# Kernel optimization log

Measured on AMD Instinct MI355X. Metric: run time of the kernel, lower is better.

## Reference

```python
import jax, jax.numpy as jnp
import numpy as np

N, M, E, DIM = 100000, 2000, 400000, 128
GIN = 2 * DIM + 3  # gate MLP input width


def _mlp2(x, W1, b1, W2, b2):
    # Linear -> ReLU -> Linear
    return jnp.maximum(x @ W1 + b1, 0.0) @ W2 + b2


def setup_inputs() -> dict:
    key = jax.random.key(0)
    ks = jax.random.split(key, 20)
    s = lambda fan_in: 1.0 / np.sqrt(fan_in)
    inp = {
        "res_feat": jax.random.normal(ks[0], (N, DIM), jnp.float32),
        "meta_feat": jax.random.normal(ks[1], (M, DIM), jnp.float32),
        "sec_ids": jax.random.randint(ks[2], (N,), 0, M),
        "batch_pe_vector": jax.random.normal(ks[3], (N, 3), jnp.float32),
        "batch_meta_2_node_edge": jax.random.randint(ks[4], (2, E), 0, M),
        "batch_meta_2_node_vector": jax.random.normal(ks[5], (E, 3), jnp.float32),
        # gate1 params
        "g1_W1": jax.random.uniform(ks[6], (GIN, DIM), jnp.float32, -s(GIN), s(GIN)),
        "g1_b1": jnp.zeros((DIM,), jnp.float32),
        "g1_W2": jax.random.uniform(ks[7], (DIM, DIM), jnp.float32, -s(DIM), s(DIM)),
        "g1_b2": jnp.zeros((DIM,), jnp.float32),
        # gate2 params
        "g2_W1": jax.random.uniform(ks[8], (GIN, DIM), jnp.float32, -s(GIN), s(GIN)),
        "g2_b1": jnp.zeros((DIM,), jnp.float32),
        "g2_W2": jax.random.uniform(ks[9], (DIM, DIM), jnp.float32, -s(DIM), s(DIM)),
        "g2_b2": jnp.zeros((DIM,), jnp.float32),
        # fuse params
        "f_W1": jax.random.uniform(ks[10], (DIM, DIM), jnp.float32, -s(DIM), s(DIM)),
        "f_b1": jnp.zeros((DIM,), jnp.float32),
        "f_W2": jax.random.uniform(ks[11], (DIM, DIM), jnp.float32, -s(DIM), s(DIM)),
        "f_b2": jnp.zeros((DIM,), jnp.float32),
    }
    return inp


def reference(res_feat, meta_feat, sec_ids, batch_pe_vector,
              batch_meta_2_node_edge, batch_meta_2_node_vector,
              g1_W1, g1_b1, g1_W2, g1_b2,
              g2_W1, g2_b1, g2_W2, g2_b2,
              f_W1, f_b1, f_W2, f_b2):
    n = res_feat.shape[0]
    # gate1: per-node gather of meta features
    meta_broadcast = meta_feat[sec_ids]                       # [N, dim]
    gate1_in = jnp.concatenate([res_feat, meta_broadcast, -batch_pe_vector], axis=-1)
    gate1_w = _mlp2(gate1_in, g1_W1, g1_b1, g1_W2, g1_b2)     # [N, dim]
    # gate2: per-edge gathers
    src, dst = batch_meta_2_node_edge[0], batch_meta_2_node_edge[1]
    meta_add = meta_feat[src]                                 # [E, dim]
    res_b = res_feat[dst]                                     # [E, dim]
    gate2_in = jnp.concatenate([res_b, meta_add, batch_meta_2_node_vector], axis=-1)
    gate2_w = _mlp2(gate2_in, g2_W1, g2_b1, g2_W2, g2_b2)     # [E, dim]
    # scatter_mean over destination nodes
    vals = gate2_w * meta_add
    sums = jax.ops.segment_sum(vals, dst, num_segments=n)
    cnts = jax.ops.segment_sum(jnp.ones((vals.shape[0],), vals.dtype), dst, num_segments=n)
    meta_add_fea = sums / jnp.maximum(cnts, 1.0)[:, None]
    fused = res_feat + gate1_w * meta_broadcast + meta_add_fea
    return _mlp2(fused, f_W1, f_b1, f_W2, f_b2)
```

## Files before the change

kernel.cpp:

```cpp
#include <hip/hip_runtime.h>


typedef short bf16x8 __attribute__((ext_vector_type(8)));
typedef float f32x4  __attribute__((ext_vector_type(4)));

#define XS_PAD 136

__device__ __forceinline__ unsigned short f2bf(float f){
  union { float f; unsigned u; } v; v.f = f;
  return (unsigned short)((v.u + 0x7FFFu + ((v.u >> 16) & 1u)) >> 16);
}
__device__ __forceinline__ unsigned pack2(float a, float b){
  return (unsigned)f2bf(a) | ((unsigned)f2bf(b) << 16);
}

__device__ __forceinline__ void mfma_layer(const unsigned short* Xs,
                                           const bf16x8 (&B)[2][4],
                                           int lane, f32x4 (&acc)[4][2]) {
  const int lcol = lane & 15, quad = lane >> 4;
  #pragma unroll
  for (int rg = 0; rg < 4; ++rg) {
    bf16x8 A[4];
    const unsigned short* ab = Xs + (rg*16 + lcol)*XS_PAD + quad*8;
    #pragma unroll
    for (int kk = 0; kk < 4; ++kk) A[kk] = *(const bf16x8*)(ab + kk*32);
    #pragma unroll
    for (int ctl = 0; ctl < 2; ++ctl)
      #pragma unroll
      for (int kk = 0; kk < 4; ++kk)
        acc[rg][ctl] = __builtin_amdgcn_mfma_f32_16x16x32_bf16(
            A[kk], B[ctl][kk], acc[rg][ctl], 0, 0, 0);
  }
}

__device__ __forceinline__ void load_bfrags(const unsigned short* __restrict__ Wt,
                                            int wave, int lane, bf16x8 (&B)[2][4]) {
  const int lcol = lane & 15, quad = lane >> 4;
  #pragma unroll
  for (int ctl = 0; ctl < 2; ++ctl) {
    int col = (wave*2 + ctl)*16 + lcol;
    #pragma unroll
    for (int kk = 0; kk < 4; ++kk)
      B[ctl][kk] = *(const bf16x8*)(Wt + (size_t)col*128 + kk*32 + quad*8);
  }
}

__device__ __forceinline__ void zero_acc(f32x4 (&acc)[4][2]) {
  #pragma unroll
  for (int rg = 0; rg < 4; ++rg)
    #pragma unroll
    for (int ctl = 0; ctl < 2; ++ctl) {
      acc[rg][ctl][0]=0.f; acc[rg][ctl][1]=0.f;
      acc[rg][ctl][2]=0.f; acc[rg][ctl][3]=0.f;
    }
}

struct WPtrs { const float* s[8]; };
__global__ __launch_bounds__(256) void transpose_w8(WPtrs p,
                                                    unsigned short* __restrict__ dstbase,
                                                    int* __restrict__ counts, int M) {
  int slab = blockIdx.x >> 4, blk = blockIdx.x & 15;
  const float* W = p.s[slab];
  unsigned short* Wt = dstbase + (size_t)slab*16384;
  int c  = blk*8 + (threadIdx.x >> 5);
  int k0 = (threadIdx.x & 31) * 4;
  unsigned short o[4];
  #pragma unroll
  for (int j = 0; j < 4; ++j) o[j] = f2bf(W[(size_t)(k0 + j)*128 + c]);
  *(uint2*)(Wt + (size_t)c*128 + k0) =
      make_uint2((unsigned)o[0] | ((unsigned)o[1] << 16),
                 (unsigned)o[2] | ((unsigned)o[3] << 16));
  int tid = blockIdx.x*256 + threadIdx.x;
  int tot = gridDim.x*256;
  for (int i = tid; i < M; i += tot) counts[i] = 0;
}

__global__ __launch_bounds__(256) void prep_and_hist(
    const float* __restrict__ res, const float* __restrict__ meta,
    const unsigned short* __restrict__ WAt, const unsigned short* __restrict__ WBt,
    const float* __restrict__ b1,
    float* __restrict__ A2, float* __restrict__ M2, int mrows, int nbPrep,
    const int* __restrict__ dst, int* __restrict__ counts, int E) {
  if ((int)blockIdx.x >= nbPrep) {
    int e = ((int)blockIdx.x - nbPrep)*256 + threadIdx.x;
    if (e < E) atomicAdd(&counts[dst[e]], 1);
    return;
  }
  __shared__ __align__(16) unsigned short Xs[64*XS_PAD];
  const int t = threadIdx.x, lane = t & 63, wave = t >> 6;
  const int quad = lane >> 4, lcol = lane & 15;
  const int half = nbPrep >> 1;
  const int yy = ((int)blockIdx.x >= half) ? 1 : 0;
  const int bx = (int)blockIdx.x - yy*half;
  const int tile0 = bx * 64;
  const float* X = yy ? meta : res;
  const unsigned short* Wt = yy ? WBt : WAt;
  float* Y = yy ? M2 : A2;
  bf16x8 B[2][4];
  load_bfrags(Wt, wave, lane, B);
  #pragma unroll
  for (int i = 0; i < 8; ++i) {
    int f = t + i*256, row = f >> 5, c4 = f & 31;
    int gr = tile0 + row;
    float4 v = make_float4(0.f,0.f,0.f,0.f);
    if (gr < mrows) v = *(const float4*)(X + (size_t)gr*128 + c4*4);
    *(uint2*)(Xs + row*XS_PAD + c4*4) = make_uint2(pack2(v.x,v.y), pack2(v.z,v.w));
  }
  __syncthreads();
  f32x4 acc[4][2]; zero_acc(acc);
  mfma_layer(Xs, B, lane, acc);
  #pragma unroll
  for (int rg = 0; rg < 4; ++rg)
    #pragma unroll
    for (int ctl = 0; ctl < 2; ++ctl) {
      int col = (wave*2 + ctl)*16 + lcol;
      float badd = 0.f;
      if (!yy) badd = b1[col];
      #pragma unroll
      for (int reg = 0; reg < 4; ++reg) {
        int gr = tile0 + rg*16 + quad*4 + reg;
        if (gr < mrows) Y[(size_t)gr*128 + col] = acc[rg][ctl][reg] + badd;
      }
    }
}

__global__ __launch_bounds__(1024) void scan_all(const int* __restrict__ counts,
                                                 int* __restrict__ row_start,
                                                 int* __restrict__ cursor, int M) {
  __shared__ int s[1024];
  __shared__ int carry_s;
  const int t = threadIdx.x;
  if (t == 0) carry_s = 0;
  __syncthreads();
  for (int base = 0; base < M; base += 2048) {
    int i0 = base + 2*t, i1 = i0 + 1;
    int c0 = (i0 < M) ? counts[i0] : 0;
    int c1 = (i1 < M) ? counts[i1] : 0;
    int pair = c0 + c1;
    s[t] = pair; __syncthreads();
    for (int off = 1; off < 1024; off <<= 1) {
      int x = (t >= off) ? s[t-off] : 0; __syncthreads();
      s[t] += x; __syncthreads();
    }
    int carry = carry_s;
    int excl = carry + s[t] - pair;
    if (i0 < M) { row_start[i0] = excl;       cursor[i0] = excl; }
    if (i1 < M) { row_start[i1] = excl + c0;  cursor[i1] = excl + c0; }
    __syncthreads();
    if (t == 1023) carry_s = carry + s[1023];
    __syncthreads();
  }
}

__global__ void fill_kernel(const int* __restrict__ dst, const int* __restrict__ src,
                            const float* __restrict__ evec, int* __restrict__ cursor,
                            float4* __restrict__ edata, int E) {
  int e = blockIdx.x*256 + threadIdx.x;
  if (e < E) {
    int p = atomicAdd(&cursor[dst[e]], 1);
    edata[p] = make_float4(__int_as_float(src[e]),
                           evec[(size_t)e*3], evec[(size_t)e*3+1], evec[(size_t)e*3+2]);
  }
}

__global__ __launch_bounds__(256) void edge_mfma(
    const float* __restrict__ A2, const float* __restrict__ M2,
    const float* __restrict__ meta, const float4* __restrict__ edata,
    const int* __restrict__ row_start, const int* __restrict__ counts,
    const float* __restrict__ g2W1full,
    const unsigned short* __restrict__ W2t, const float* __restrict__ b2,
    float* __restrict__ SUM) {
  const int n = blockIdx.x;
  const int cnt = counts[n];
  if (cnt <= 0) return;
  const int rs = row_start[n];

  __shared__ __align__(16) unsigned short Xh[64*XS_PAD];
  __shared__ int srcl[64];
  __shared__ float evl[192];
  const int t = threadIdx.x, lane = t & 63, wave = t >> 6;
  const int quad = lane >> 4, lcol = lane & 15;
  const int c0 = (t & 31) * 4, rbase = t >> 5;

  float4 ed = make_float4(0.f,0.f,0.f,0.f);
  if (t < 64 && t < cnt) ed = edata[rs + t];

  bf16x8 BW2[2][4];
  load_bfrags(W2t, wave, lane, BW2);
  float4 base = *(const float4*)(A2 + (size_t)n*128 + c0);
  float4 w0 = *(const float4*)(g2W1full + 256*128 + c0);
  float4 w1 = *(const float4*)(g2W1full + 257*128 + c0);
  float4 w2 = *(const float4*)(g2W1full + 258*128 + c0);
  const int colA = wave*32 + lcol, colB = colA + 16;
  const float b2A = b2[colA], b2B = b2[colB];
  float psA = 0.f, psB = 0.f;

  for (int t0 = 0; t0 < cnt; t0 += 64) {
    if (t0) __syncthreads();
    if (t < 64) {
      srcl[t] = __float_as_int(ed.x);
      evl[3*t] = ed.y; evl[3*t+1] = ed.z; evl[3*t+2] = ed.w;
      int idx = t0 + 64 + t;
      ed = make_float4(0.f,0.f,0.f,0.f);
      if (idx < cnt) ed = edata[rs + idx];
    }
    __syncthreads();
    #pragma unroll
    for (int i = 0; i < 8; ++i) {
      int row = rbase + 8*i;
      float4 h = make_float4(0.f,0.f,0.f,0.f);
      if (t0 + row < cnt) {
        int s = srcl[row];
        float4 m = *(const float4*)(M2 + (size_t)s*128 + c0);
        float e0 = evl[3*row], e1 = evl[3*row+1], e2 = evl[3*row+2];
        h.x = fmaxf(base.x + m.x + e0*w0.x + e1*w1.x + e2*w2.x, 0.f);
        h.y = fmaxf(base.y + m.y + e0*w0.y + e1*w1.y + e2*w2.y, 0.f);
        h.z = fmaxf(base.z + m.z + e0*w0.z + e1*w1.z + e2*w2.z, 0.f);
        h.w = fmaxf(base.w + m.w + e0*w0.w + e1*w1.w + e2*w2.w, 0.f);
      }
      *(uint2*)(Xh + row*XS_PAD + c0) = make_uint2(pack2(h.x,h.y), pack2(h.z,h.w));
    }
    __syncthreads();
    f32x4 acc[4][2]; zero_acc(acc);
    mfma_layer(Xh, BW2, lane, acc);
    #pragma unroll
    for (int rg = 0; rg < 4; ++rg)
      #pragma unroll
      for (int reg = 0; reg < 4; ++reg) {
        int rl = rg*16 + quad*4 + reg;
        if (t0 + rl < cnt) {
          int s = srcl[rl];
          psA += (acc[rg][0][reg] + b2A) * meta[(size_t)s*128 + colA];
          psB += (acc[rg][1][reg] + b2B) * meta[(size_t)s*128 + colB];
        }
      }
  }
  psA += __shfl_xor(psA, 16, 64); psA += __shfl_xor(psA, 32, 64);
  psB += __shfl_xor(psB, 16, 64); psB += __shfl_xor(psB, 32, 64);
  if (quad == 0) {
    SUM[(size_t)n*128 + colA] = psA;
    SUM[(size_t)n*128 + colB] = psB;
  }
}

__global__ __launch_bounds__(256) void fused_node(
    const float* __restrict__ res, const float* __restrict__ meta,
    const int* __restrict__ sec_ids, const float* __restrict__ pe,
    const float* __restrict__ g1W1full,
    const unsigned short* __restrict__ g1At, const unsigned short* __restrict__ g1Bt,
    const unsigned short* __restrict__ g1W2t, const float* __restrict__ g1b1,
    const float* __restrict__ g1b2,
    const unsigned short* __restrict__ fW1t, const float* __restrict__ fb1v,
    const unsigned short* __restrict__ fW2t, const float* __restrict__ fb2v,
    const float* __restrict__ SUM, const int* __restrict__ counts, int msize,
    float* __restrict__ out, int rows) {
  __shared__ __align__(16) unsigned short Xs[64*XS_PAD];
  __shared__ int   sids[64];
  __shared__ float pel[192];
  __shared__ float inv[64];
  const int t = threadIdx.x, lane = t & 63, wave = t >> 6;
  const int quad = lane >> 4, lcol = lane & 15;
  const int tile0 = blockIdx.x * 64;
  const int c0 = (t & 31) * 4, rbase = t >> 5;
  const int colA = wave*32 + lcol, colB = colA + 16;

  if (t < 64) {
    int gr = tile0 + t;
    sids[t] = (gr < rows) ? sec_ids[gr] : 0;
    float p0=0.f,p1=0.f,p2=0.f;
    if (gr < rows){ p0=pe[(size_t)gr*3]; p1=pe[(size_t)gr*3+1]; p2=pe[(size_t)gr*3+2]; }
    pel[3*t]=p0; pel[3*t+1]=p1; pel[3*t+2]=p2;
    int c = (gr < rows && gr < msize) ? counts[gr] : 0;
    inv[t] = (c > 0) ? 1.f/(float)c : 0.f;
  }
  bf16x8 BF[2][4];
  load_bfrags(g1At, wave, lane, BF);
  #pragma unroll
  for (int i = 0; i < 8; ++i) {
    int row = rbase + 8*i, gr = tile0 + row;
    float4 v = make_float4(0.f,0.f,0.f,0.f);
    if (gr < rows) v = *(const float4*)(res + (size_t)gr*128 + c0);
    *(uint2*)(Xs + row*XS_PAD + c0) = make_uint2(pack2(v.x,v.y), pack2(v.z,v.w));
  }
  __syncthreads();
  f32x4 acc[4][2]; zero_acc(acc);
  mfma_layer(Xs, BF, lane, acc);
  load_bfrags(g1Bt, wave, lane, BF);
  __syncthreads();
  #pragma unroll
  for (int i = 0; i < 8; ++i) {
    int row = rbase + 8*i, gr = tile0 + row;
    float4 v = make_float4(0.f,0.f,0.f,0.f);
    if (gr < rows) v = *(const float4*)(meta + (size_t)sids[row]*128 + c0);
    *(uint2*)(Xs + row*XS_PAD + c0) = make_uint2(pack2(v.x,v.y), pack2(v.z,v.w));
  }
  __syncthreads();
  mfma_layer(Xs, BF, lane, acc);
  load_bfrags(g1W2t, wave, lane, BF);
  __syncthreads();
  {
    const float b1A = g1b1[colA], b1B = g1b1[colB];
    const float wA0 = g1W1full[256*128+colA], wA1 = g1W1full[257*128+colA],
                wA2 = g1W1full[258*128+colA];
    const float wB0 = g1W1full[256*128+colB], wB1 = g1W1full[257*128+colB],
                wB2 = g1W1full[258*128+colB];
    #pragma unroll
    for (int rg = 0; rg < 4; ++rg)
      #pragma unroll
      for (int reg = 0; reg < 4; ++reg) {
        int row = rg*16 + quad*4 + reg;
        float p0 = pel[3*row], p1 = pel[3*row+1], p2 = pel[3*row+2];
        float vA = acc[rg][0][reg] + b1A - p0*wA0 - p1*wA1 - p2*wA2;
        float vB = acc[rg][1][reg] + b1B - p0*wB0 - p1*wB1 - p2*wB2;
        Xs[row*XS_PAD + colA] = f2bf(fmaxf(vA, 0.f));
        Xs[row*XS_PAD + colB] = f2bf(fmaxf(vB, 0.f));
      }
  }
  __syncthreads();
  zero_acc(acc);
  mfma_layer(Xs, BF, lane, acc);
  load_bfrags(fW1t, wave, lane, BF);
  __syncthreads();
  {
    const float b2A = g1b2[colA], b2B = g1b2[colB];
    #pragma unroll
    for (int rg = 0; rg < 4; ++rg)
      #pragma unroll
      for (int reg = 0; reg < 4; ++reg) {
        int row = rg*16 + quad*4 + reg, gr = tile0 + row;
        unsigned short oA = 0, oB = 0;
        if (gr < rows) {
          int sid = sids[row];
          float gA = acc[rg][0][reg] + b2A, gB = acc[rg][1][reg] + b2B;
          float mA = meta[(size_t)sid*128 + colA], mB = meta[(size_t)sid*128 + colB];
          float rA = res[(size_t)gr*128 + colA],  rB = res[(size_t)gr*128 + colB];
          float iv = inv[row];
          float sA = 0.f, sB = 0.f;
          if (iv > 0.f) {
            sA = SUM[(size_t)gr*128 + colA] * iv;
            sB = SUM[(size_t)gr*128 + colB] * iv;
          }
          oA = f2bf(rA + gA*mA + sA);
          oB = f2bf(rB + gB*mB + sB);
        }
        Xs[row*XS_PAD + colA] = oA;
        Xs[row*XS_PAD + colB] = oB;
      }
  }
  __syncthreads();
  zero_acc(acc);
  mfma_layer(Xs, BF, lane, acc);
  load_bfrags(fW2t, wave, lane, BF);
  __syncthreads();
  {
    const float fb1A = fb1v[colA], fb1B = fb1v[colB];
    #pragma unroll
    for (int rg = 0; rg < 4; ++rg)
      #pragma unroll
      for (int reg = 0; reg < 4; ++reg) {
        int row = rg*16 + quad*4 + reg;
        Xs[row*XS_PAD + colA] = f2bf(fmaxf(acc[rg][0][reg] + fb1A, 0.f));
        Xs[row*XS_PAD + colB] = f2bf(fmaxf(acc[rg][1][reg] + fb1B, 0.f));
      }
  }
  __syncthreads();
  zero_acc(acc);
  mfma_layer(Xs, BF, lane, acc);
  {
    const float fb2A = fb2v[colA], fb2B = fb2v[colB];
    #pragma unroll
    for (int rg = 0; rg < 4; ++rg)
      #pragma unroll
      for (int reg = 0; reg < 4; ++reg) {
        int gr = tile0 + rg*16 + quad*4 + reg;
        if (gr < rows) {
          out[(size_t)gr*128 + colA] = acc[rg][0][reg] + fb2A;
          out[(size_t)gr*128 + colB] = acc[rg][1][reg] + fb2B;
        }
      }
  }
}

extern "C" void kernel_launch(void* const* d_in, const int* in_sizes, int n_in,
                              void* d_out, int out_size, void* d_ws, size_t ws_size,
                              hipStream_t stream) {
  const float* res     = (const float*)d_in[0];
  const float* meta    = (const float*)d_in[1];
  const int*   sec_ids = (const int*)  d_in[2];
  const float* pe      = (const float*)d_in[3];
  const int*   edge    = (const int*)  d_in[4];
  const float* evec    = (const float*)d_in[5];
  const float* g1W1 = (const float*)d_in[6];
  const float* g1b1 = (const float*)d_in[7];
  const float* g1W2 = (const float*)d_in[8];
  const float* g1b2 = (const float*)d_in[9];
  const float* g2W1 = (const float*)d_in[10];
  const float* g2b1 = (const float*)d_in[11];
  const float* g2W2 = (const float*)d_in[12];
  const float* g2b2 = (const float*)d_in[13];
  const float* fW1  = (const float*)d_in[14];
  const float* fb1  = (const float*)d_in[15];
  const float* fW2  = (const float*)d_in[16];
  const float* fb2  = (const float*)d_in[17];

  const int N = in_sizes[0] / 128;
  const int M = in_sizes[1] / 128;
  const int E = in_sizes[4] / 2;
  const int* src = edge;
  const int* dst = edge + E;

  float* ws = (float*)d_ws;
  float* A2   = ws;
  float* M2   = A2 + (size_t)M*128;
  float* SUMb = M2 + (size_t)M*128;
  int* counts     = (int*)(SUMb + (size_t)M*128);
  int* row_startp = counts + M;
  int* cursor     = row_startp + M;
  uintptr_t ap = (uintptr_t)(cursor + M);
  ap = (ap + 15) & ~(uintptr_t)15;
  float4* edata = (float4*)ap;
  uintptr_t wp = (uintptr_t)(edata + E);
  wp = (wp + 15) & ~(uintptr_t)15;
  unsigned short* Wt = (unsigned short*)wp;
  unsigned short* W_g1A  = Wt + 0*16384;
  unsigned short* W_g1B  = Wt + 1*16384;
  unsigned short* W_g1W2 = Wt + 2*16384;
  unsigned short* W_g2A  = Wt + 3*16384;
  unsigned short* W_g2B  = Wt + 4*16384;
  unsigned short* W_g2W2 = Wt + 5*16384;
  unsigned short* W_fW1  = Wt + 6*16384;
  unsigned short* W_fW2  = Wt + 7*16384;
  float* out = (float*)d_out;

  WPtrs p;
  p.s[0] = g1W1;            p.s[1] = g1W1 + 128*128;  p.s[2] = g1W2;
  p.s[3] = g2W1;            p.s[4] = g2W1 + 128*128;  p.s[5] = g2W2;
  p.s[6] = fW1;             p.s[7] = fW2;

  const int nbMt = (M + 63) / 64;
  const int nbN  = (N + 63) / 64;
  const int nbE  = (E + 255) / 256;
  const int nbPrep = 2*nbMt;

  transpose_w8<<<128, 256, 0, stream>>>(p, Wt, counts, M);
  prep_and_hist<<<nbPrep + nbE, 256, 0, stream>>>(res, meta, W_g2A, W_g2B, g2b1,
                                                  A2, M2, M, nbPrep, dst, counts, E);
  scan_all<<<1, 1024, 0, stream>>>(counts, row_startp, cursor, M);
  fill_kernel<<<nbE, 256, 0, stream>>>(dst, src, evec, cursor, edata, E);
  edge_mfma<<<M, 256, 0, stream>>>(A2, M2, meta, edata, row_startp, counts,
                                   g2W1, W_g2W2, g2b2, SUMb);
  fused_node<<<nbN, 256, 0, stream>>>(res, meta, sec_ids, pe, g1W1,
                                      W_g1A, W_g1B, W_g1W2, g1b1, g1b2,
                                      W_fW1, fb1, W_fW2, fb2,
                                      SUMb, counts, M, out, N);
}
```

Baseline: 382.4 us.

## Co-schedule edge and node-tile work in one launch and merge prep stages

The pipeline is reorganised so the histogram runs alongside the weight transpose, and the edge fill runs alongside the A2/M2 projection. The counts buffer is now zeroed with an explicit memset. The edge kernel and most node tiles are merged into one interleaved launch; only node tiles whose SUM rows depend on edge results (index below M) are deferred to a tail kernel. The aim is to cut launch count and idle time between small kernels by overlapping independent work, at the cost of shared-memory union overhead and some dispatch complexity.

```diff
diff --git a/kernel.cpp b/kernel.cpp
--- a/kernel.cpp
+++ b/kernel.cpp
@@ -5,6 +5,8 @@
 typedef float f32x4  __attribute__((ext_vector_type(4)));
 
 #define XS_PAD 136
+#define XS_BYTES (64*XS_PAD*2)
+#define SMEM_BYTES 18944
 
 __device__ __forceinline__ unsigned short f2bf(float f){
   union { float f; unsigned u; } v; v.f = f;
@@ -56,10 +58,17 @@
 }
 
 struct WPtrs { const float* s[8]; };
-__global__ __launch_bounds__(256) void transpose_w8(WPtrs p,
-                                                    unsigned short* __restrict__ dstbase,
-                                                    int* __restrict__ counts, int M) {
-  int slab = blockIdx.x >> 4, blk = blockIdx.x & 15;
+__global__ __launch_bounds__(256) void transpose_hist(WPtrs p,
+                                                      unsigned short* __restrict__ dstbase,
+                                                      const int* __restrict__ dst,
+                                                      int* __restrict__ counts, int E) {
+  int bid = blockIdx.x;
+  if (bid >= 128) {
+    int e = (bid - 128)*256 + threadIdx.x;
+    if (e < E) atomicAdd(&counts[dst[e]], 1);
+    return;
+  }
+  int slab = bid >> 4, blk = bid & 15;
   const float* W = p.s[slab];
   unsigned short* Wt = dstbase + (size_t)slab*16384;
   int c  = blk*8 + (threadIdx.x >> 5);
@@ -70,58 +79,6 @@
   *(uint2*)(Wt + (size_t)c*128 + k0) =
       make_uint2((unsigned)o[0] | ((unsigned)o[1] << 16),
                  (unsigned)o[2] | ((unsigned)o[3] << 16));
-  int tid = blockIdx.x*256 + threadIdx.x;
-  int tot = gridDim.x*256;
-  for (int i = tid; i < M; i += tot) counts[i] = 0;
-}
-
-__global__ __launch_bounds__(256) void prep_and_hist(
-    const float* __restrict__ res, const float* __restrict__ meta,
-    const unsigned short* __restrict__ WAt, const unsigned short* __restrict__ WBt,
-    const float* __restrict__ b1,
-    float* __restrict__ A2, float* __restrict__ M2, int mrows, int nbPrep,
-    const int* __restrict__ dst, int* __restrict__ counts, int E) {
-  if ((int)blockIdx.x >= nbPrep) {
-    int e = ((int)blockIdx.x - nbPrep)*256 + threadIdx.x;
-    if (e < E) atomicAdd(&counts[dst[e]], 1);
-    return;
-  }
-  __shared__ __align__(16) unsigned short Xs[64*XS_PAD];
-  const int t = threadIdx.x, lane = t & 63, wave = t >> 6;
-  const int quad = lane >> 4, lcol = lane & 15;
-  const int half = nbPrep >> 1;
-  const int yy = ((int)blockIdx.x >= half) ? 1 : 0;
-  const int bx = (int)blockIdx.x - yy*half;
-  const int tile0 = bx * 64;
-  const float* X = yy ? meta : res;
-  const unsigned short* Wt = yy ? WBt : WAt;
-  float* Y = yy ? M2 : A2;
-  bf16x8 B[2][4];
-  load_bfrags(Wt, wave, lane, B);
-  #pragma unroll
-  for (int i = 0; i < 8; ++i) {
-    int f = t + i*256, row = f >> 5, c4 = f & 31;
-    int gr = tile0 + row;
-    float4 v = make_float4(0.f,0.f,0.f,0.f);
-    if (gr < mrows) v = *(const float4*)(X + (size_t)gr*128 + c4*4);
-    *(uint2*)(Xs + row*XS_PAD + c4*4) = make_uint2(pack2(v.x,v.y), pack2(v.z,v.w));
-  }
-  __syncthreads();
-  f32x4 acc[4][2]; zero_acc(acc);
-  mfma_layer(Xs, B, lane, acc);
-  #pragma unroll
-  for (int rg = 0; rg < 4; ++rg)
-    #pragma unroll
-    for (int ctl = 0; ctl < 2; ++ctl) {
-      int col = (wave*2 + ctl)*16 + lcol;
-      float badd = 0.f;
-      if (!yy) badd = b1[col];
-      #pragma unroll
-      for (int reg = 0; reg < 4; ++reg) {
-        int gr = tile0 + rg*16 + quad*4 + reg;
-        if (gr < mrows) Y[(size_t)gr*128 + col] = acc[rg][ctl][reg] + badd;
-      }
-    }
 }
 
 __global__ __launch_bounds__(1024) void scan_all(const int* __restrict__ counts,
@@ -152,32 +109,76 @@
   }
 }
 
-__global__ void fill_kernel(const int* __restrict__ dst, const int* __restrict__ src,
-                            const float* __restrict__ evec, int* __restrict__ cursor,
-                            float4* __restrict__ edata, int E) {
-  int e = blockIdx.x*256 + threadIdx.x;
-  if (e < E) {
-    int p = atomicAdd(&cursor[dst[e]], 1);
-    edata[p] = make_float4(__int_as_float(src[e]),
-                           evec[(size_t)e*3], evec[(size_t)e*3+1], evec[(size_t)e*3+2]);
-  }
-}
-
-__global__ __launch_bounds__(256) void edge_mfma(
+__global__ __launch_bounds__(256) void prep_fill(
+    const float* __restrict__ res, const float* __restrict__ meta,
+    const unsigned short* __restrict__ WAt, const unsigned short* __restrict__ WBt,
+    const float* __restrict__ b1,
+    float* __restrict__ A2, float* __restrict__ M2, int mrows, int nbPrep,
+    const int* __restrict__ dst, const int* __restrict__ src,
+    const float* __restrict__ evec, int* __restrict__ cursor,
+    float4* __restrict__ edata, int E) {
+  if ((int)blockIdx.x >= nbPrep) {
+    int e = ((int)blockIdx.x - nbPrep)*256 + threadIdx.x;
+    if (e < E) {
+      int pp = atomicAdd(&cursor[dst[e]], 1);
+      edata[pp] = make_float4(__int_as_float(src[e]),
+                              evec[(size_t)e*3], evec[(size_t)e*3+1], evec[(size_t)e*3+2]);
+    }
+    return;
+  }
+  __shared__ __align__(16) unsigned short Xs[64*XS_PAD];
+  const int t = threadIdx.x, lane = t & 63, wave = t >> 6;
+  const int quad = lane >> 4, lcol = lane & 15;
+  const int half = nbPrep >> 1;
+  const int yy = ((int)blockIdx.x >= half) ? 1 : 0;
+  const int bx = (int)blockIdx.x - yy*half;
+  const int tile0 = bx * 64;
+  const float* X = yy ? meta : res;
+  const unsigned short* Wt = yy ? WBt : WAt;
+  float* Y = yy ? M2 : A2;
+  bf16x8 B[2][4];
+  load_bfrags(Wt, wave, lane, B);
+  #pragma unroll
+  for (int i = 0; i < 8; ++i) {
+    int f = t + i*256, row = f >> 5, c4 = f & 31;
+    int gr = tile0 + row;
+    float4 v = make_float4(0.f,0.f,0.f,0.f);
+    if (gr < mrows) v = *(const float4*)(X + (size_t)gr*128 + c4*4);
+    *(uint2*)(Xs + row*XS_PAD + c4*4) = make_uint2(pack2(v.x,v.y), pack2(v.z,v.w));
+  }
+  __syncthreads();
+  f32x4 acc[4][2]; zero_acc(acc);
+  mfma_layer(Xs, B, lane, acc);
+  #pragma unroll
+  for (int rg = 0; rg < 4; ++rg)
+    #pragma unroll
+    for (int ctl = 0; ctl < 2; ++ctl) {
+      int col = (wave*2 + ctl)*16 + lcol;
+      float badd = 0.f;
+      if (!yy) badd = b1[col];
+      #pragma unroll
+      for (int reg = 0; reg < 4; ++reg) {
+        int gr = tile0 + rg*16 + quad*4 + reg;
+        if (gr < mrows) Y[(size_t)gr*128 + col] = acc[rg][ctl][reg] + badd;
+      }
+    }
+}
+
+__device__ __forceinline__ void edge_body(
+    unsigned char* smem, int n,
     const float* __restrict__ A2, const float* __restrict__ M2,
     const float* __restrict__ meta, const float4* __restrict__ edata,
     const int* __restrict__ row_start, const int* __restrict__ counts,
     const float* __restrict__ g2W1full,
     const unsigned short* __restrict__ W2t, const float* __restrict__ b2,
     float* __restrict__ SUM) {
-  const int n = blockIdx.x;
   const int cnt = counts[n];
   if (cnt <= 0) return;
   const int rs = row_start[n];
 
-  __shared__ __align__(16) unsigned short Xh[64*XS_PAD];
-  __shared__ int srcl[64];
-  __shared__ float evl[192];
+  unsigned short* Xh  = (unsigned short*)smem;
+  int*   srcl = (int*)(smem + XS_BYTES);
+  float* evl  = (float*)(smem + XS_BYTES + 256);
   const int t = threadIdx.x, lane = t & 63, wave = t >> 6;
   const int quad = lane >> 4, lcol = lane & 15;
   const int c0 = (t & 31) * 4, rbase = t >> 5;
@@ -243,7 +244,8 @@
   }
 }
 
-__global__ __launch_bounds__(256) void fused_node(
+__device__ __forceinline__ void fused_body(
+    unsigned char* smem, int tile,
     const float* __restrict__ res, const float* __restrict__ meta,
     const int* __restrict__ sec_ids, const float* __restrict__ pe,
     const float* __restrict__ g1W1full,
@@ -254,13 +256,13 @@
     const unsigned short* __restrict__ fW2t, const float* __restrict__ fb2v,
     const float* __restrict__ SUM, const int* __restrict__ counts, int msize,
     float* __restrict__ out, int rows) {
-  __shared__ __align__(16) unsigned short Xs[64*XS_PAD];
-  __shared__ int   sids[64];
-  __shared__ float pel[192];
-  __shared__ float inv[64];
+  unsigned short* Xs  = (unsigned short*)smem;
+  int*   sids = (int*)(smem + XS_BYTES);
+  float* pel  = (float*)(smem + XS_BYTES + 256);
+  float* inv  = (float*)(smem + XS_BYTES + 1024);
   const int t = threadIdx.x, lane = t & 63, wave = t >> 6;
   const int quad = lane >> 4, lcol = lane & 15;
-  const int tile0 = blockIdx.x * 64;
+  const int tile0 = tile * 64;
   const int c0 = (t & 31) * 4, rbase = t >> 5;
   const int colA = wave*32 + lcol, colB = colA + 16;
 
@@ -379,6 +381,59 @@
         }
       }
   }
+}
+
+__global__ __launch_bounds__(256) void edge_fused(
+    const float* __restrict__ A2, const float* __restrict__ M2,
+    const float* __restrict__ meta, const float4* __restrict__ edata,
+    const int* __restrict__ row_start, const int* __restrict__ counts,
+    const float* __restrict__ g2W1full,
+    const unsigned short* __restrict__ W2t, const float* __restrict__ g2b2v,
+    float* __restrict__ SUM,
+    const float* __restrict__ res, const int* __restrict__ sec_ids,
+    const float* __restrict__ pe, const float* __restrict__ g1W1full,
+    const unsigned short* __restrict__ g1At, const unsigned short* __restrict__ g1Bt,
+    const unsigned short* __restrict__ g1W2t, const float* __restrict__ g1b1,
+    const float* __restrict__ g1b2,
+    const unsigned short* __restrict__ fW1t, const float* __restrict__ fb1v,
+    const unsigned short* __restrict__ fW2t, const float* __restrict__ fb2v,
+    int msize, float* __restrict__ out, int rows,
+    int nEdge, int nFused, int splitTile) {
+  __shared__ __align__(16) unsigned char smem[SMEM_BYTES];
+  const int bid = blockIdx.x;
+  const int minEF = (nEdge < nFused) ? nEdge : nFused;
+  const int paired = 2*minEF;
+  int isEdge, id;
+  if (bid < paired) { isEdge = ((bid & 1) == 0); id = bid >> 1; }
+  else {
+    int r = bid - paired;
+    if (nEdge > nFused) { isEdge = 1; id = nFused + r; }
+    else                { isEdge = 0; id = nEdge + r; }
+  }
+  if (isEdge)
+    edge_body(smem, id, A2, M2, meta, edata, row_start, counts,
+              g2W1full, W2t, g2b2v, SUM);
+  else
+    fused_body(smem, splitTile + id, res, meta, sec_ids, pe, g1W1full,
+               g1At, g1Bt, g1W2t, g1b1, g1b2, fW1t, fb1v, fW2t, fb2v,
+               SUM, counts, msize, out, rows);
+}
+
+__global__ __launch_bounds__(256) void fused_tail(
+    const float* __restrict__ res, const float* __restrict__ meta,
+    const int* __restrict__ sec_ids, const float* __restrict__ pe,
+    const float* __restrict__ g1W1full,
+    const unsigned short* __restrict__ g1At, const unsigned short* __restrict__ g1Bt,
+    const unsigned short* __restrict__ g1W2t, const float* __restrict__ g1b1,
+    const float* __restrict__ g1b2,
+    const unsigned short* __restrict__ fW1t, const float* __restrict__ fb1v,
+    const unsigned short* __restrict__ fW2t, const float* __restrict__ fb2v,
+    const float* __restrict__ SUM, const int* __restrict__ counts, int msize,
+    float* __restrict__ out, int rows) {
+  __shared__ __align__(16) unsigned char smem[SMEM_BYTES];
+  fused_body(smem, blockIdx.x, res, meta, sec_ids, pe, g1W1full,
+             g1At, g1Bt, g1W2t, g1b1, g1b2, fW1t, fb1v, fW2t, fb2v,
+             SUM, counts, msize, out, rows);
 }
 
 extern "C" void kernel_launch(void* const* d_in, const int* in_sizes, int n_in,
@@ -437,20 +492,29 @@
   p.s[3] = g2W1;            p.s[4] = g2W1 + 128*128;  p.s[5] = g2W2;
   p.s[6] = fW1;             p.s[7] = fW2;
 
-  const int nbMt = (M + 63) / 64;
-  const int nbN  = (N + 63) / 64;
-  const int nbE  = (E + 255) / 256;
+  const int nbMt   = (M + 63) / 64;
+  const int nbN    = (N + 63) / 64;
+  const int nbE    = (E + 255) / 256;
   const int nbPrep = 2*nbMt;
-
-  transpose_w8<<<128, 256, 0, stream>>>(p, Wt, counts, M);
-  prep_and_hist<<<nbPrep + nbE, 256, 0, stream>>>(res, meta, W_g2A, W_g2B, g2b1,
-                                                  A2, M2, M, nbPrep, dst, counts, E);
+  int splitTile = (M + 63) / 64;
+  if (splitTile > nbN) splitTile = nbN;
+  const int nFused = nbN - splitTile;
+
+  hipMemsetAsync(counts, 0, (size_t)M*sizeof(int), stream);
+  transpose_hist<<<128 + nbE, 256, 0, stream>>>(p, Wt, dst, counts, E);
   scan_all<<<1, 1024, 0, stream>>>(counts, row_startp, cursor, M);
-  fill_kernel<<<nbE, 256, 0, stream>>>(dst, src, evec, cursor, edata, E);
-  edge_mfma<<<M, 256, 0, stream>>>(A2, M2, meta, edata, row_startp, counts,
-                                   g2W1, W_g2W2, g2b2, SUMb);
-  fused_node<<<nbN, 256, 0, stream>>>(res, meta, sec_ids, pe, g1W1,
-                                      W_g1A, W_g1B, W_g1W2, g1b1, g1b2,
-                                      W_fW1, fb1, W_fW2, fb2,
-                                      SUMb, counts, M, out, N);
-}
+  prep_fill<<<nbPrep + nbE, 256, 0, stream>>>(res, meta, W_g2A, W_g2B, g2b1,
+                                              A2, M2, M, nbPrep,
+                                              dst, src, evec, cursor, edata, E);
+  edge_fused<<<M + nFused, 256, 0, stream>>>(A2, M2, meta, edata, row_startp, counts,
+                                             g2W1, W_g2W2, g2b2, SUMb,
+                                             res, sec_ids, pe, g1W1,
+                                             W_g1A, W_g1B, W_g1W2, g1b1, g1b2,
+                                             W_fW1, fb1, W_fW2, fb2,
+                                             M, out, N, M, nFused, splitTile);
+  if (splitTile > 0)
+    fused_tail<<<splitTile, 256, 0, stream>>>(res, meta, sec_ids, pe, g1W1,
+                                              W_g1A, W_g1B, W_g1W2, g1b1, g1b2,
+                                              W_fW1, fb1, W_fW2, fb2,
+                                              SUMb, counts, M, out, N);
+}
```

New measurement: 431.0 us. +12.7%, slower.

## Precompute gate1 meta projection per meta row instead of per node

Applied to the files above, without the earlier changes.

The meta_feat slice of gate1's first layer (meta @ W1B) is now computed once per meta row (M=2000) in the prep kernel into a new M1 buffer. The node kernel gathers M1[sec_id] and adds it in the epilogue instead of gathering meta rows into LDS and running a second MFMA layer per node tile. This removes one 128x128 matmul per node and one LDS staging pass, in exchange for scattered float reads of M1 in the epilogue and extra prep blocks. Numerics change slightly because M1 is accumulated from bf16 inputs and then kept in fp32.

```diff
diff --git a/kernel.cpp b/kernel.cpp
--- a/kernel.cpp
+++ b/kernel.cpp
@@ -78,8 +78,9 @@
 __global__ __launch_bounds__(256) void prep_and_hist(
     const float* __restrict__ res, const float* __restrict__ meta,
     const unsigned short* __restrict__ WAt, const unsigned short* __restrict__ WBt,
-    const float* __restrict__ b1,
-    float* __restrict__ A2, float* __restrict__ M2, int mrows, int nbPrep,
+    const unsigned short* __restrict__ WCt, const float* __restrict__ b1,
+    float* __restrict__ A2, float* __restrict__ M2, float* __restrict__ M1,
+    int mrows, int nbPrep,
     const int* __restrict__ dst, int* __restrict__ counts, int E) {
   if ((int)blockIdx.x >= nbPrep) {
     int e = ((int)blockIdx.x - nbPrep)*256 + threadIdx.x;
@@ -89,13 +90,13 @@
   __shared__ __align__(16) unsigned short Xs[64*XS_PAD];
   const int t = threadIdx.x, lane = t & 63, wave = t >> 6;
   const int quad = lane >> 4, lcol = lane & 15;
-  const int half = nbPrep >> 1;
-  const int yy = ((int)blockIdx.x >= half) ? 1 : 0;
-  const int bx = (int)blockIdx.x - yy*half;
+  const int third = nbPrep / 3;
+  const int yy = (int)blockIdx.x / third;
+  const int bx = (int)blockIdx.x - yy*third;
   const int tile0 = bx * 64;
-  const float* X = yy ? meta : res;
-  const unsigned short* Wt = yy ? WBt : WAt;
-  float* Y = yy ? M2 : A2;
+  const float* X = (yy == 0) ? res : meta;
+  const unsigned short* Wt = (yy == 0) ? WAt : (yy == 1) ? WBt : WCt;
+  float* Y = (yy == 0) ? A2 : (yy == 1) ? M2 : M1;
   bf16x8 B[2][4];
   load_bfrags(Wt, wave, lane, B);
   #pragma unroll
@@ -115,7 +116,7 @@
     for (int ctl = 0; ctl < 2; ++ctl) {
       int col = (wave*2 + ctl)*16 + lcol;
       float badd = 0.f;
-      if (!yy) badd = b1[col];
+      if (yy == 0) badd = b1[col];
       #pragma unroll
       for (int reg = 0; reg < 4; ++reg) {
         int gr = tile0 + rg*16 + quad*4 + reg;
@@ -246,8 +247,8 @@
 __global__ __launch_bounds__(256) void fused_node(
     const float* __restrict__ res, const float* __restrict__ meta,
     const int* __restrict__ sec_ids, const float* __restrict__ pe,
-    const float* __restrict__ g1W1full,
-    const unsigned short* __restrict__ g1At, const unsigned short* __restrict__ g1Bt,
+    const float* __restrict__ g1W1full, const float* __restrict__ M1,
+    const unsigned short* __restrict__ g1At,
     const unsigned short* __restrict__ g1W2t, const float* __restrict__ g1b1,
     const float* __restrict__ g1b2,
     const unsigned short* __restrict__ fW1t, const float* __restrict__ fb1v,
@@ -285,17 +286,6 @@
   __syncthreads();
   f32x4 acc[4][2]; zero_acc(acc);
   mfma_layer(Xs, BF, lane, acc);
-  load_bfrags(g1Bt, wave, lane, BF);
-  __syncthreads();
-  #pragma unroll
-  for (int i = 0; i < 8; ++i) {
-    int row = rbase + 8*i, gr = tile0 + row;
-    float4 v = make_float4(0.f,0.f,0.f,0.f);
-    if (gr < rows) v = *(const float4*)(meta + (size_t)sids[row]*128 + c0);
-    *(uint2*)(Xs + row*XS_PAD + c0) = make_uint2(pack2(v.x,v.y), pack2(v.z,v.w));
-  }
-  __syncthreads();
-  mfma_layer(Xs, BF, lane, acc);
   load_bfrags(g1W2t, wave, lane, BF);
   __syncthreads();
   {
@@ -309,9 +299,12 @@
       #pragma unroll
       for (int reg = 0; reg < 4; ++reg) {
         int row = rg*16 + quad*4 + reg;
+        int sid = sids[row];
+        float m1A = M1[(size_t)sid*128 + colA];
+        float m1B = M1[(size_t)sid*128 + colB];
         float p0 = pel[3*row], p1 = pel[3*row+1], p2 = pel[3*row+2];
-        float vA = acc[rg][0][reg] + b1A - p0*wA0 - p1*wA1 - p2*wA2;
-        float vB = acc[rg][1][reg] + b1B - p0*wB0 - p1*wB1 - p2*wB2;
+        float vA = acc[rg][0][reg] + m1A + b1A - p0*wA0 - p1*wA1 - p2*wA2;
+        float vB = acc[rg][1][reg] + m1B + b1B - p0*wB0 - p1*wB1 - p2*wB2;
         Xs[row*XS_PAD + colA] = f2bf(fmaxf(vA, 0.f));
         Xs[row*XS_PAD + colB] = f2bf(fmaxf(vB, 0.f));
       }
@@ -412,7 +405,8 @@
   float* ws = (float*)d_ws;
   float* A2   = ws;
   float* M2   = A2 + (size_t)M*128;
-  float* SUMb = M2 + (size_t)M*128;
+  float* M1   = M2 + (size_t)M*128;
+  float* SUMb = M1 + (size_t)M*128;
   int* counts     = (int*)(SUMb + (size_t)M*128);
   int* row_startp = counts + M;
   int* cursor     = row_startp + M;
@@ -437,20 +431,21 @@
   p.s[3] = g2W1;            p.s[4] = g2W1 + 128*128;  p.s[5] = g2W2;
   p.s[6] = fW1;             p.s[7] = fW2;
 
-  const int nbMt = (M + 63) / 64;
-  const int nbN  = (N + 63) / 64;
-  const int nbE  = (E + 255) / 256;
-  const int nbPrep = 2*nbMt;
+  const int nbMt   = (M + 63) / 64;
+  const int nbN    = (N + 63) / 64;
+  const int nbE    = (E + 255) / 256;
+  const int nbPrep = 3*nbMt;
 
   transpose_w8<<<128, 256, 0, stream>>>(p, Wt, counts, M);
-  prep_and_hist<<<nbPrep + nbE, 256, 0, stream>>>(res, meta, W_g2A, W_g2B, g2b1,
-                                                  A2, M2, M, nbPrep, dst, counts, E);
+  prep_and_hist<<<nbPrep + nbE, 256, 0, stream>>>(res, meta, W_g2A, W_g2B, W_g1B,
+                                                  g2b1, A2, M2, M1, M, nbPrep,
+                                                  dst, counts, E);
   scan_all<<<1, 1024, 0, stream>>>(counts, row_startp, cursor, M);
   fill_kernel<<<nbE, 256, 0, stream>>>(dst, src, evec, cursor, edata, E);
   edge_mfma<<<M, 256, 0, stream>>>(A2, M2, meta, edata, row_startp, counts,
                                    g2W1, W_g2W2, g2b2, SUMb);
-  fused_node<<<nbN, 256, 0, stream>>>(res, meta, sec_ids, pe, g1W1,
-                                      W_g1A, W_g1B, W_g1W2, g1b1, g1b2,
+  fused_node<<<nbN, 256, 0, stream>>>(res, meta, sec_ids, pe, g1W1, M1,
+                                      W_g1A, W_g1W2, g1b1, g1b2,
                                       W_fW1, fb1, W_fW2, fb2,
                                       SUMb, counts, M, out, N);
 }
```

After: 375.3 us. About the same (-1.9%).
